# Optimization experiments

Measured on AMD Instinct MI355X. Metric: run time of the kernel, lower is better.

Reference implementation:

```python
import jax, jax.numpy as jnp
import numpy as np

B = 64          # graphs per batch
NPG = 4000      # nodes per graph
CPG0 = 400      # level-0 clusters per graph
CPG1 = 40       # level-1 clusters per graph
DEG = 8         # avg degree
F_IN = 64       # node feature dim (input_shape)


def setup_inputs() -> dict:
    rng = np.random.RandomState(0)
    N0 = B * NPG
    E0 = N0 * DEG
    N1 = B * CPG0
    N2 = B * CPG1
    # node -> graph and node -> level-0 cluster (globally consecutive ids)
    node_graph = np.repeat(np.arange(N0 // NPG), NPG)
    local = np.tile(np.arange(NPG), B)
    cluster0 = node_graph * CPG0 + local // (NPG // CPG0)
    # random edges, endpoints within the same graph
    edge_graph = np.repeat(np.arange(B), NPG * DEG)
    src = edge_graph * NPG + rng.randint(0, NPG, size=E0)
    dst = edge_graph * NPG + rng.randint(0, NPG, size=E0)
    edge_index = np.stack([src, dst]).astype(np.int64)
    # community_pooling's pool_edge: map edges through cluster0, drop self-loops,
    # coalesce duplicates (edge_attr summed). Precompute the integer structure.
    ci, cj = cluster0[src], cluster0[dst]
    mask = ci != cj
    key_ = ci.astype(np.int64) * N1 + cj.astype(np.int64)
    uniq, inv = np.unique(key_[mask], return_inverse=True)
    E1 = uniq.shape[0]
    edge_seg = np.full(E0, E1, dtype=np.int64)   # dropped self-loops -> dummy seg E1
    edge_seg[mask] = inv
    edge_index1 = np.stack([uniq // N1, uniq % N1]).astype(np.int64)
    # level-1 clusters on pooled nodes and graph id of each level-1 cluster
    cl_idx = np.arange(N1)
    cluster1 = (cl_idx // CPG0) * CPG1 + (cl_idx % CPG0) // (CPG0 // CPG1)
    batch2 = np.arange(N2) // CPG1

    key = jax.random.key(0)
    ks = jax.random.split(key, 10)

    def lin(k, fin, fout):
        return jax.random.normal(k, (fin, fout), jnp.float32) / np.sqrt(fin)

    return dict(
        x=jax.random.normal(ks[0], (N0, F_IN), jnp.float32),
        edge_attr=jax.random.uniform(ks[1], (E0, 1), jnp.float32),
        edge_index=jnp.asarray(edge_index),
        cluster0=jnp.asarray(cluster0.astype(np.int64)),
        edge_index1=jnp.asarray(edge_index1),
        edge_seg=jnp.asarray(edge_seg),
        cluster1=jnp.asarray(cluster1.astype(np.int64)),
        batch2=jnp.asarray(batch2.astype(np.int64)),
        n_clusters0=N1, n_clusters1=N2, n_graphs=B,
        W1=lin(ks[2], F_IN, 16), We1=lin(ks[3], 1, 1), Wa1=lin(ks[4], 2 * 16 + 1, 1),
        W2=lin(ks[5], 16, 32), We2=lin(ks[6], 1, 1), Wa2=lin(ks[7], 2 * 32 + 1, 1),
        fc1_W=lin(ks[8], 32, 64), fc1_b=jnp.zeros((64,), jnp.float32),
        fc2_W=lin(ks[9], 64, 1), fc2_b=jnp.zeros((1,), jnp.float32),
    )


def _gin_conv(x, edge_index, edge_attr, W, We, Wa, num_nodes):
    # DeepRank-GNN GINetConvLayer (all linears bias-free)
    row, col = edge_index[0], edge_index[1]
    xp = x @ W                      # project once, then gather (same math as fc(x[col]))
    xrow, xcol = xp[row], xp[col]   # (E, out)
    ed = edge_attr @ We             # (E, n_edge_feat)
    alpha = jnp.concatenate([xrow, xcol, ed], axis=1) @ Wa   # (E, 1)
    alpha = jax.nn.leaky_relu(alpha)
    # faithful: softmax over dim=1 of an (E,1) tensor -> all ones
    alpha = jax.nn.softmax(alpha, axis=1)
    h = alpha * xcol
    return jax.ops.segment_sum(h, row, num_segments=num_nodes)


def reference(x, edge_attr, edge_index, cluster0, edge_index1, edge_seg,
              cluster1, batch2, n_clusters0, n_clusters1, n_graphs,
              W1, We1, Wa1, W2, We2, Wa2, fc1_W, fc1_b, fc2_W, fc2_b):
    # conv1 + relu
    x1 = jax.nn.relu(_gin_conv(x, edge_index, edge_attr, W1, We1, Wa1, x.shape[0]))
    # community_pooling: scatter_max nodes onto clusters, coalesced pooled edges
    x_pool = jax.ops.segment_max(x1, cluster0, num_segments=n_clusters0)
    E1 = edge_index1.shape[1]
    ea1 = jax.ops.segment_sum(edge_attr, edge_seg, num_segments=E1 + 1)[:E1]
    # conv2 + relu on pooled graph
    x2 = jax.nn.relu(_gin_conv(x_pool, edge_index1, ea1, W2, We2, Wa2, n_clusters0))
    # max_pool_x over level-1 clusters, then scatter_mean per graph
    x3 = jax.ops.segment_max(x2, cluster1, num_segments=n_clusters1)
    s = jax.ops.segment_sum(x3, batch2, num_segments=n_graphs)
    cnt = jax.ops.segment_sum(jnp.ones((x3.shape[0], 1), x3.dtype), batch2,
                              num_segments=n_graphs)
    xg = s / cnt                                  # (B, 32)
    h = jax.nn.relu(xg @ fc1_W + fc1_b)           # (B, 64)
    return h @ fc2_W + fc2_b                      # (B, 1)
```

## Files before the change

### kernel.cpp

```cpp
#include <hip/hip_runtime.h>
#include <hip/hip_bf16.h>


#define C1 16
#define C2 32
#define NPG 4000
#define EPG 32000
#define P   8
#define EPP (EPG / P)
#define RPB 80

__global__ void gemm1_k(const float* __restrict__ x, const float* __restrict__ W,
                        float* __restrict__ xp1, int N0) {
    int n = blockIdx.x * blockDim.x + threadIdx.x;
    if (n >= N0) return;
    const float4* xr = (const float4*)(x + (size_t)n * 64);
    float acc[C1];
#pragma unroll
    for (int j = 0; j < C1; ++j) acc[j] = 0.f;
#pragma unroll
    for (int k4 = 0; k4 < 16; ++k4) {
        float4 v = xr[k4];
        const float* w0 = W + (k4 * 4 + 0) * C1;
        const float* w1 = W + (k4 * 4 + 1) * C1;
        const float* w2 = W + (k4 * 4 + 2) * C1;
        const float* w3 = W + (k4 * 4 + 3) * C1;
#pragma unroll
        for (int j = 0; j < C1; ++j)
            acc[j] += v.x * w0[j] + v.y * w1[j] + v.z * w2[j] + v.w * w3[j];
    }
    float4* o = (float4*)(xp1 + (size_t)n * C1);
#pragma unroll
    for (int q = 0; q < 4; ++q)
        o[q] = make_float4(acc[4 * q], acc[4 * q + 1], acc[4 * q + 2], acc[4 * q + 3]);
}

__global__ __launch_bounds__(1024) void csr0_k(const int* __restrict__ ei,
                                               int* __restrict__ rp0,
                                               int* __restrict__ scol,
                                               int E0, int B) {
    __shared__ int cnt[NPG];
    __shared__ int tsum[1024];
    int g = blockIdx.x % B;
    int p = blockIdx.x / B;
    int t = threadIdx.x;
    const int* rows = ei + (size_t)g * EPG + p * EPP;
    const int* cols = ei + E0 + (size_t)g * EPG + p * EPP;
    int rbase = g * NPG;
    int ebase = g * EPG + p * EPP;
    int* rpp = rp0 + (size_t)(p * B + g) * (NPG + 1);

    for (int i = t; i < NPG; i += 1024) cnt[i] = 0;
    __syncthreads();
    for (int e = t; e < EPP; e += 1024) atomicAdd(&cnt[rows[e] - rbase], 1);
    __syncthreads();

    int loc[4];
    int s = 0;
#pragma unroll
    for (int k = 0; k < 4; ++k) {
        int idx = 4 * t + k;
        int v = (idx < NPG) ? cnt[idx] : 0;
        loc[k] = s;
        s += v;
    }
    tsum[t] = s;
    __syncthreads();
    int mine = s;
    for (int off = 1; off < 1024; off <<= 1) {
        int u = (t >= off) ? tsum[t - off] : 0;
        __syncthreads();
        tsum[t] += u;
        __syncthreads();
    }
    int excl = tsum[t] - mine;
#pragma unroll
    for (int k = 0; k < 4; ++k) {
        int idx = 4 * t + k;
        if (idx < NPG) {
            int pos = excl + loc[k];
            rpp[idx] = ebase + pos;
            cnt[idx] = pos;
        }
    }
    if (t == 1023) rpp[NPG] = ebase + EPP;
    __syncthreads();

    for (int e = t; e < EPP; e += 1024) {
        int r = rows[e] - rbase;
        int c = cols[e];
        int pos = atomicAdd(&cnt[r], 1);
        scol[ebase + pos] = c;
    }
}

__global__ __launch_bounds__(256) void merge_k(const int* __restrict__ rp0,
                                               const int* __restrict__ scol,
                                               int* __restrict__ rp2,
                                               int* __restrict__ scol2,
                                               int B, int N0, int E0) {
    int g = blockIdx.x % B;
    int cb = blockIdx.x / B;
    int t = threadIdx.x;
    if (blockIdx.x == 0 && t == 0) rp2[N0] = E0;
    int rl = cb * 256 + t;
    if (rl >= NPG) return;
    int r = g * NPG + rl;
    int s0[P], cnt[P];
    int sum = 0;
#pragma unroll
    for (int p = 0; p < P; ++p) {
        const int* rpp = rp0 + (size_t)(p * B + g) * (NPG + 1) + rl;
        int a = rpp[0];
        int b = rpp[1];
        s0[p] = a;
        cnt[p] = b - a;
        sum += a;
    }
    int base = sum - (P - 1) * g * EPG - EPP * (P * (P - 1) / 2);
    rp2[r] = base;
    int wpos[P];
    int w = base;
#pragma unroll
    for (int p = 0; p < P; ++p) { wpos[p] = w; w += cnt[p]; }
#pragma unroll
    for (int p = 0; p < P; ++p)
        if (cnt[p] > 0) scol2[wpos[p]] = scol[s0[p]];
#pragma unroll
    for (int p = 0; p < P; ++p)
        for (int k = 1; k < cnt[p]; ++k)
            scol2[wpos[p] + k] = scol[s0[p] + k];
}

__global__ __launch_bounds__(320) void aggell_k(const int* __restrict__ rp2,
                                                const int* __restrict__ scol2,
                                                const float* __restrict__ xp1,
                                                float* __restrict__ xpool,
                                                int B, int cpg) {
    __shared__ float4 sums[RPB][4];
    int g = blockIdx.x % B;
    int cb = blockIdx.x / B;
    int t = threadIdx.x;
    int f4 = t & 3;
    int rl = t >> 2;
    int r = g * NPG + cb * RPB + rl;
    int e0 = rp2[r];
    int cnt = rp2[r + 1] - e0;
    const float4* xp = (const float4*)xp1;
    float4 s = make_float4(0.f, 0.f, 0.f, 0.f);
#pragma unroll
    for (int k = 0; k < 16; ++k) {
        if (k < cnt) {
            float4 v = xp[(size_t)scol2[e0 + k] * 4 + f4];
            s.x += v.x; s.y += v.y; s.z += v.z; s.w += v.w;
        }
    }
    for (int k = 16; k < cnt; ++k) {
        float4 v = xp[(size_t)scol2[e0 + k] * 4 + f4];
        s.x += v.x; s.y += v.y; s.z += v.z; s.w += v.w;
    }
    sums[rl][f4] = s;
    __syncthreads();
    if (t < 32) {
        int cl = t >> 2, ff = t & 3;
        float4 m = sums[cl * 10][ff];
#pragma unroll
        for (int k = 1; k < 10; ++k) {
            float4 v = sums[cl * 10 + k][ff];
            m.x = fmaxf(m.x, v.x); m.y = fmaxf(m.y, v.y);
            m.z = fmaxf(m.z, v.z); m.w = fmaxf(m.w, v.w);
        }
        m.x = fmaxf(m.x, 0.f); m.y = fmaxf(m.y, 0.f);
        m.z = fmaxf(m.z, 0.f); m.w = fmaxf(m.w, 0.f);
        ((float4*)xpool)[(size_t)(g * cpg + cb * 8 + cl) * 4 + ff] = m;
    }
}

__global__ void rowptr_k(const int* __restrict__ ei1, int* __restrict__ rp, int E1, int N1) {
    int e = blockIdx.x * blockDim.x + threadIdx.x;
    if (e >= E1) return;
    int r = ei1[e];
    int rprev = __shfl_up(r, 1);
    if ((threadIdx.x & 63) == 0) rprev = (e == 0) ? -1 : ei1[e - 1];
    for (int rr = rprev + 1; rr <= r; ++rr) rp[rr] = e;
    if (e == E1 - 1)
        for (int rr = r + 1; rr <= N1; ++rr) rp[rr] = E1;
}

__global__ __launch_bounds__(256) void agg2_k(const int* __restrict__ ei1,
                                              const int* __restrict__ rp,
                                              const float* __restrict__ xpool,
                                              const float* __restrict__ W2,
                                              float* __restrict__ x2acc,
                                              int E1, int B, int cpg) {
    __shared__ float sums[4][C1];
    int g = blockIdx.x % B;
    int c = blockIdx.x / B;
    int t = threadIdx.x;
    int f4 = t & 3;
    int es = (t >> 2) & 15;
    int w = t >> 6;
    int r = g * cpg + c * 4 + w;
    const int* col = ei1 + E1;
    float4 acc = make_float4(0.f, 0.f, 0.f, 0.f);
    int e0 = rp[r], e1e = rp[r + 1];
    for (int e = e0 + es; e < e1e; e += 16) {
        float4 v = ((const float4*)(xpool + (size_t)col[e] * C1))[f4];
        acc.x += v.x; acc.y += v.y; acc.z += v.z; acc.w += v.w;
    }
#pragma unroll
    for (int off = 4; off <= 32; off <<= 1) {
        acc.x += __shfl_xor(acc.x, off);
        acc.y += __shfl_xor(acc.y, off);
        acc.z += __shfl_xor(acc.z, off);
        acc.w += __shfl_xor(acc.w, off);
    }
    if (es == 0) {
        sums[w][f4 * 4 + 0] = acc.x;
        sums[w][f4 * 4 + 1] = acc.y;
        sums[w][f4 * 4 + 2] = acc.z;
        sums[w][f4 * 4 + 3] = acc.w;
    }
    __syncthreads();
    if (t < 128) {
        int w2 = t >> 5, j = t & 31;
        const float* s = sums[w2];
        float v = 0.f;
#pragma unroll
        for (int k = 0; k < C1; ++k) v += s[k] * W2[k * C2 + j];
        x2acc[(size_t)(g * cpg + c * 4 + w2) * C2 + j] = v;
    }
}

__global__ __launch_bounds__(256) void final_k(const float* __restrict__ x2acc,
                                               const float* __restrict__ fc1W,
                                               const float* __restrict__ fc1b,
                                               const float* __restrict__ fc2W,
                                               const float* __restrict__ fc2b,
                                               float* __restrict__ out, int cpg) {
    __shared__ float xgs[C2];
    int g = blockIdx.x;
    int t = threadIdx.x;
    if (t < C2) xgs[t] = 0.f;
    __syncthreads();
    for (int i = t; i < 40 * C2; i += 256) {
        int cl = i >> 5, f = i & 31;
        const float* base = x2acc + ((size_t)g * cpg + cl * 10) * C2 + f;
        float m = base[0];
#pragma unroll
        for (int k = 1; k < 10; ++k) m = fmaxf(m, base[k * C2]);
        atomicAdd(&xgs[f], fmaxf(m, 0.f));
    }
    __syncthreads();
    if (t < 64) {
        float h = fc1b[t];
#pragma unroll
        for (int f = 0; f < C2; ++f) h += xgs[f] * (1.f / 40.f) * fc1W[f * 64 + t];
        h = fmaxf(h, 0.f);
        float v = h * fc2W[t];
#pragma unroll
        for (int off = 32; off > 0; off >>= 1) v += __shfl_down(v, off);
        if (t == 0) out[g] = v + fc2b[0];
    }
}

extern "C" void kernel_launch(void* const* d_in, const int* in_sizes, int n_in,
                              void* d_out, int out_size, void* d_ws, size_t ws_size,
                              hipStream_t stream) {
    const float* x    = (const float*)d_in[0];
    const int*   ei   = (const int*)d_in[2];
    const int*   ei1  = (const int*)d_in[4];
    const float* W1   = (const float*)d_in[11];
    const float* W2   = (const float*)d_in[14];
    const float* fc1W = (const float*)d_in[17];
    const float* fc1b = (const float*)d_in[18];
    const float* fc2W = (const float*)d_in[19];
    const float* fc2b = (const float*)d_in[20];
    float* out = (float*)d_out;

    const int N0 = in_sizes[0] / 64;
    const int E0 = in_sizes[2] / 2;
    const int E1 = in_sizes[4] / 2;
    const int N1 = in_sizes[6];
    const int N2 = in_sizes[7];
    const int B  = N2 / 40;
    const int CPG0 = N1 / B;

    float* xp1   = (float*)d_ws;
    float* xpool = xp1 + (size_t)N0 * C1;
    float* x2acc = xpool + (size_t)N1 * C1;
    int*   rp1   = (int*)(x2acc + (size_t)N1 * C2);
    int*   rp0   = rp1 + (N1 + 2);
    int*   scol  = rp0 + (size_t)B * P * (NPG + 1) + 2;
    int*   scol2 = scol + (size_t)E0;
    int*   rp2   = scol2 + (size_t)E0;

    gemm1_k<<<(N0 + 255) / 256, 256, 0, stream>>>(x, W1, xp1, N0);
    csr0_k<<<B * P, 1024, 0, stream>>>(ei, rp0, scol, E0, B);
    merge_k<<<B * ((NPG + 255) / 256), 256, 0, stream>>>(rp0, scol, rp2, scol2, B, N0, E0);
    aggell_k<<<B * (NPG / RPB), 320, 0, stream>>>(rp2, scol2, xp1, xpool, B, CPG0);
    rowptr_k<<<(E1 + 255) / 256, 256, 0, stream>>>(ei1, rp1, E1, N1);
    agg2_k<<<B * (CPG0 / 4), 256, 0, stream>>>(ei1, rp1, xpool, W2, x2acc, E1, B, CPG0);
    final_k<<<B, 256, 0, stream>>>(x2acc, fc1W, fc1b, fc2W, fc2b, out, CPG0);
}
```

Before: 256.8 us.

## Replace per-graph CSR build and merge with fixed-width ELL using global atomics

The two-pass CSR construction (per-partition shared-memory counting sort, block-wide scan, then a merge kernel) is replaced by a single ELL build. Each edge atomically claims a slot in a global per-row counter and writes its graph-local column as a 16-bit index into a 32-wide row. The first GEMM, zeroing the counters and the level-1 row-pointer build are fused into one multi-role launch, and the aggregation kernel reads the ELL rows directly. This removes the scan, the merge pass and two launches, and shrinks the column index traffic. In exchange, rows with more than 32 neighbours silently lose edges, which is safe only while degrees stay small. The atomic slot order also makes the order of summation nondeterministic.

```diff
diff --git a/kernel.cpp b/kernel.cpp
--- a/kernel.cpp
+++ b/kernel.cpp
@@ -1,139 +1,85 @@
 #include <hip/hip_runtime.h>
-#include <hip/hip_bf16.h>
 
 
 #define C1 16
 #define C2 32
 #define NPG 4000
 #define EPG 32000
-#define P   8
-#define EPP (EPG / P)
+#define ELLW 32
+#define PB2 16
 #define RPB 80
 
-__global__ void gemm1_k(const float* __restrict__ x, const float* __restrict__ W,
-                        float* __restrict__ xp1, int N0) {
-    int n = blockIdx.x * blockDim.x + threadIdx.x;
-    if (n >= N0) return;
-    const float4* xr = (const float4*)(x + (size_t)n * 64);
-    float acc[C1];
-#pragma unroll
-    for (int j = 0; j < C1; ++j) acc[j] = 0.f;
-#pragma unroll
-    for (int k4 = 0; k4 < 16; ++k4) {
-        float4 v = xr[k4];
-        const float* w0 = W + (k4 * 4 + 0) * C1;
-        const float* w1 = W + (k4 * 4 + 1) * C1;
-        const float* w2 = W + (k4 * 4 + 2) * C1;
-        const float* w3 = W + (k4 * 4 + 3) * C1;
-#pragma unroll
-        for (int j = 0; j < C1; ++j)
-            acc[j] += v.x * w0[j] + v.y * w1[j] + v.z * w2[j] + v.w * w3[j];
-    }
-    float4* o = (float4*)(xp1 + (size_t)n * C1);
-#pragma unroll
-    for (int q = 0; q < 4; ++q)
-        o[q] = make_float4(acc[4 * q], acc[4 * q + 1], acc[4 * q + 2], acc[4 * q + 3]);
-}
-
-__global__ __launch_bounds__(1024) void csr0_k(const int* __restrict__ ei,
-                                               int* __restrict__ rp0,
-                                               int* __restrict__ scol,
-                                               int E0, int B) {
-    __shared__ int cnt[NPG];
-    __shared__ int tsum[1024];
+__global__ __launch_bounds__(256) void pre_k(const float* __restrict__ x,
+                                             const float* __restrict__ W,
+                                             float* __restrict__ xp1,
+                                             int* __restrict__ cnt,
+                                             const int* __restrict__ ei1,
+                                             int* __restrict__ rp,
+                                             int N0, int E1, int N1,
+                                             int G1, int ZB) {
+    int bid = blockIdx.x;
+    int t = threadIdx.x;
+    if (bid < G1) {
+        int n = bid * 256 + t;
+        if (n >= N0) return;
+        const float4* xr = (const float4*)(x + (size_t)n * 64);
+        float acc[C1];
+#pragma unroll
+        for (int j = 0; j < C1; ++j) acc[j] = 0.f;
+#pragma unroll
+        for (int k4 = 0; k4 < 16; ++k4) {
+            float4 v = xr[k4];
+            const float* w0 = W + (k4 * 4 + 0) * C1;
+            const float* w1 = W + (k4 * 4 + 1) * C1;
+            const float* w2 = W + (k4 * 4 + 2) * C1;
+            const float* w3 = W + (k4 * 4 + 3) * C1;
+#pragma unroll
+            for (int j = 0; j < C1; ++j)
+                acc[j] += v.x * w0[j] + v.y * w1[j] + v.z * w2[j] + v.w * w3[j];
+        }
+        float4* o = (float4*)(xp1 + (size_t)n * C1);
+#pragma unroll
+        for (int q = 0; q < 4; ++q)
+            o[q] = make_float4(acc[4 * q], acc[4 * q + 1], acc[4 * q + 2], acc[4 * q + 3]);
+    } else if (bid < G1 + ZB) {
+        int4* p = (int4*)cnt;
+        int n4 = N0 >> 2;
+        for (int i = (bid - G1) * 256 + t; i < n4; i += ZB * 256)
+            p[i] = make_int4(0, 0, 0, 0);
+    } else {
+        int e = (bid - G1 - ZB) * 256 + t;
+        if (e >= E1) return;
+        int r = ei1[e];
+        int rprev = __shfl_up(r, 1);
+        if ((t & 63) == 0) rprev = (e == 0) ? -1 : ei1[e - 1];
+        for (int rr = rprev + 1; rr <= r; ++rr) rp[rr] = e;
+        if (e == E1 - 1)
+            for (int rr = r + 1; rr <= N1; ++rr) rp[rr] = E1;
+    }
+}
+
+__global__ __launch_bounds__(256) void ell_k(const int* __restrict__ ei,
+                                             int* __restrict__ cnt,
+                                             unsigned short* __restrict__ ell,
+                                             int E0, int B) {
     int g = blockIdx.x % B;
     int p = blockIdx.x / B;
     int t = threadIdx.x;
-    const int* rows = ei + (size_t)g * EPG + p * EPP;
-    const int* cols = ei + E0 + (size_t)g * EPG + p * EPP;
+    const int EPB = EPG / PB2;
+    const int* rows = ei + (size_t)g * EPG + p * EPB;
+    const int* cols = ei + E0 + (size_t)g * EPG + p * EPB;
     int rbase = g * NPG;
-    int ebase = g * EPG + p * EPP;
-    int* rpp = rp0 + (size_t)(p * B + g) * (NPG + 1);
-
-    for (int i = t; i < NPG; i += 1024) cnt[i] = 0;
-    __syncthreads();
-    for (int e = t; e < EPP; e += 1024) atomicAdd(&cnt[rows[e] - rbase], 1);
-    __syncthreads();
-
-    int loc[4];
-    int s = 0;
-#pragma unroll
-    for (int k = 0; k < 4; ++k) {
-        int idx = 4 * t + k;
-        int v = (idx < NPG) ? cnt[idx] : 0;
-        loc[k] = s;
-        s += v;
-    }
-    tsum[t] = s;
-    __syncthreads();
-    int mine = s;
-    for (int off = 1; off < 1024; off <<= 1) {
-        int u = (t >= off) ? tsum[t - off] : 0;
-        __syncthreads();
-        tsum[t] += u;
-        __syncthreads();
-    }
-    int excl = tsum[t] - mine;
-#pragma unroll
-    for (int k = 0; k < 4; ++k) {
-        int idx = 4 * t + k;
-        if (idx < NPG) {
-            int pos = excl + loc[k];
-            rpp[idx] = ebase + pos;
-            cnt[idx] = pos;
-        }
-    }
-    if (t == 1023) rpp[NPG] = ebase + EPP;
-    __syncthreads();
-
-    for (int e = t; e < EPP; e += 1024) {
-        int r = rows[e] - rbase;
-        int c = cols[e];
+    for (int e = t; e < EPB; e += 256) {
+        int r = rows[e];
+        unsigned short c = (unsigned short)(cols[e] - rbase);
         int pos = atomicAdd(&cnt[r], 1);
-        scol[ebase + pos] = c;
-    }
-}
-
-__global__ __launch_bounds__(256) void merge_k(const int* __restrict__ rp0,
-                                               const int* __restrict__ scol,
-                                               int* __restrict__ rp2,
-                                               int* __restrict__ scol2,
-                                               int B, int N0, int E0) {
-    int g = blockIdx.x % B;
-    int cb = blockIdx.x / B;
-    int t = threadIdx.x;
-    if (blockIdx.x == 0 && t == 0) rp2[N0] = E0;
-    int rl = cb * 256 + t;
-    if (rl >= NPG) return;
-    int r = g * NPG + rl;
-    int s0[P], cnt[P];
-    int sum = 0;
-#pragma unroll
-    for (int p = 0; p < P; ++p) {
-        const int* rpp = rp0 + (size_t)(p * B + g) * (NPG + 1) + rl;
-        int a = rpp[0];
-        int b = rpp[1];
-        s0[p] = a;
-        cnt[p] = b - a;
-        sum += a;
-    }
-    int base = sum - (P - 1) * g * EPG - EPP * (P * (P - 1) / 2);
-    rp2[r] = base;
-    int wpos[P];
-    int w = base;
-#pragma unroll
-    for (int p = 0; p < P; ++p) { wpos[p] = w; w += cnt[p]; }
-#pragma unroll
-    for (int p = 0; p < P; ++p)
-        if (cnt[p] > 0) scol2[wpos[p]] = scol[s0[p]];
-#pragma unroll
-    for (int p = 0; p < P; ++p)
-        for (int k = 1; k < cnt[p]; ++k)
-            scol2[wpos[p] + k] = scol[s0[p] + k];
-}
-
-__global__ __launch_bounds__(320) void aggell_k(const int* __restrict__ rp2,
-                                                const int* __restrict__ scol2,
+        if (pos < ELLW)
+            ell[(size_t)r * ELLW + pos] = c;
+    }
+}
+
+__global__ __launch_bounds__(320) void aggell_k(const int* __restrict__ cnt,
+                                                const unsigned short* __restrict__ ell,
                                                 const float* __restrict__ xp1,
                                                 float* __restrict__ xpool,
                                                 int B, int cpg) {
@@ -144,19 +90,20 @@
     int f4 = t & 3;
     int rl = t >> 2;
     int r = g * NPG + cb * RPB + rl;
-    int e0 = rp2[r];
-    int cnt = rp2[r + 1] - e0;
+    int c = cnt[r];
+    const unsigned short* er = ell + (size_t)r * ELLW;
+    size_t gb4 = (size_t)g * NPG * 4;
     const float4* xp = (const float4*)xp1;
     float4 s = make_float4(0.f, 0.f, 0.f, 0.f);
 #pragma unroll
     for (int k = 0; k < 16; ++k) {
-        if (k < cnt) {
-            float4 v = xp[(size_t)scol2[e0 + k] * 4 + f4];
+        if (k < c) {
+            float4 v = xp[gb4 + (size_t)er[k] * 4 + f4];
             s.x += v.x; s.y += v.y; s.z += v.z; s.w += v.w;
         }
     }
-    for (int k = 16; k < cnt; ++k) {
-        float4 v = xp[(size_t)scol2[e0 + k] * 4 + f4];
+    for (int k = 16; k < c; ++k) {
+        float4 v = xp[gb4 + (size_t)er[k] * 4 + f4];
         s.x += v.x; s.y += v.y; s.z += v.z; s.w += v.w;
     }
     sums[rl][f4] = s;
@@ -174,17 +121,6 @@
         m.z = fmaxf(m.z, 0.f); m.w = fmaxf(m.w, 0.f);
         ((float4*)xpool)[(size_t)(g * cpg + cb * 8 + cl) * 4 + ff] = m;
     }
-}
-
-__global__ void rowptr_k(const int* __restrict__ ei1, int* __restrict__ rp, int E1, int N1) {
-    int e = blockIdx.x * blockDim.x + threadIdx.x;
-    if (e >= E1) return;
-    int r = ei1[e];
-    int rprev = __shfl_up(r, 1);
-    if ((threadIdx.x & 63) == 0) rprev = (e == 0) ? -1 : ei1[e - 1];
-    for (int rr = rprev + 1; rr <= r; ++rr) rp[rr] = e;
-    if (e == E1 - 1)
-        for (int rr = r + 1; rr <= N1; ++rr) rp[rr] = E1;
 }
 
 __global__ __launch_bounds__(256) void agg2_k(const int* __restrict__ ei1,
@@ -290,16 +226,17 @@
     float* xpool = xp1 + (size_t)N0 * C1;
     float* x2acc = xpool + (size_t)N1 * C1;
     int*   rp1   = (int*)(x2acc + (size_t)N1 * C2);
-    int*   rp0   = rp1 + (N1 + 2);
-    int*   scol  = rp0 + (size_t)B * P * (NPG + 1) + 2;
-    int*   scol2 = scol + (size_t)E0;
-    int*   rp2   = scol2 + (size_t)E0;
-
-    gemm1_k<<<(N0 + 255) / 256, 256, 0, stream>>>(x, W1, xp1, N0);
-    csr0_k<<<B * P, 1024, 0, stream>>>(ei, rp0, scol, E0, B);
-    merge_k<<<B * ((NPG + 255) / 256), 256, 0, stream>>>(rp0, scol, rp2, scol2, B, N0, E0);
-    aggell_k<<<B * (NPG / RPB), 320, 0, stream>>>(rp2, scol2, xp1, xpool, B, CPG0);
-    rowptr_k<<<(E1 + 255) / 256, 256, 0, stream>>>(ei1, rp1, E1, N1);
+    int*   cnt   = rp1 + (N1 + 4);
+    unsigned short* ell = (unsigned short*)(cnt + N0);
+
+    const int G1 = (N0 + 255) / 256;
+    const int ZB = 64;
+    const int RB = (E1 + 255) / 256;
+
+    pre_k<<<G1 + ZB + RB, 256, 0, stream>>>(x, W1, xp1, cnt, ei1, rp1,
+                                            N0, E1, N1, G1, ZB);
+    ell_k<<<B * PB2, 256, 0, stream>>>(ei, cnt, ell, E0, B);
+    aggell_k<<<B * (NPG / RPB), 320, 0, stream>>>(cnt, ell, xp1, xpool, B, CPG0);
     agg2_k<<<B * (CPG0 / 4), 256, 0, stream>>>(ei1, rp1, xpool, W2, x2acc, E1, B, CPG0);
     final_k<<<B, 256, 0, stream>>>(x2acc, fc1W, fc1b, fc2W, fc2b, out, CPG0);
 }
```

Result: slower. 331.3 us (+29.0%).

## Drop CSR merge pass; aggregate directly from per-partition CSRs and fuse rowptr into gemm

Applied to the files above, without the earlier changes.

Removes the merge kernel that combined the eight per-partition CSR pieces into one CSR. The level-0 aggregation now reads the partition row pointers into shared memory and gathers neighbours from all eight pieces directly. The pooled-graph rowptr build is folded into the feature GEMM launch as extra blocks. Together this cuts two launches and a full read and write of the column array, at the cost of more irregular per-row loops in the aggregation.

```diff
diff --git a/kernel.cpp b/kernel.cpp
--- a/kernel.cpp
+++ b/kernel.cpp
@@ -1,5 +1,4 @@
 #include <hip/hip_runtime.h>
-#include <hip/hip_bf16.h>
 
 
 #define C1 16
@@ -10,29 +9,46 @@
 #define EPP (EPG / P)
 #define RPB 80
 
-__global__ void gemm1_k(const float* __restrict__ x, const float* __restrict__ W,
-                        float* __restrict__ xp1, int N0) {
-    int n = blockIdx.x * blockDim.x + threadIdx.x;
-    if (n >= N0) return;
-    const float4* xr = (const float4*)(x + (size_t)n * 64);
-    float acc[C1];
-#pragma unroll
-    for (int j = 0; j < C1; ++j) acc[j] = 0.f;
-#pragma unroll
-    for (int k4 = 0; k4 < 16; ++k4) {
-        float4 v = xr[k4];
-        const float* w0 = W + (k4 * 4 + 0) * C1;
-        const float* w1 = W + (k4 * 4 + 1) * C1;
-        const float* w2 = W + (k4 * 4 + 2) * C1;
-        const float* w3 = W + (k4 * 4 + 3) * C1;
-#pragma unroll
-        for (int j = 0; j < C1; ++j)
-            acc[j] += v.x * w0[j] + v.y * w1[j] + v.z * w2[j] + v.w * w3[j];
-    }
-    float4* o = (float4*)(xp1 + (size_t)n * C1);
-#pragma unroll
-    for (int q = 0; q < 4; ++q)
-        o[q] = make_float4(acc[4 * q], acc[4 * q + 1], acc[4 * q + 2], acc[4 * q + 3]);
+__global__ __launch_bounds__(256) void pre_k(const float* __restrict__ x,
+                                             const float* __restrict__ W,
+                                             float* __restrict__ xp1,
+                                             const int* __restrict__ ei1,
+                                             int* __restrict__ rp,
+                                             int N0, int E1, int N1, int G1) {
+    int bid = blockIdx.x;
+    int t = threadIdx.x;
+    if (bid < G1) {
+        int n = bid * 256 + t;
+        if (n >= N0) return;
+        const float4* xr = (const float4*)(x + (size_t)n * 64);
+        float acc[C1];
+#pragma unroll
+        for (int j = 0; j < C1; ++j) acc[j] = 0.f;
+#pragma unroll
+        for (int k4 = 0; k4 < 16; ++k4) {
+            float4 v = xr[k4];
+            const float* w0 = W + (k4 * 4 + 0) * C1;
+            const float* w1 = W + (k4 * 4 + 1) * C1;
+            const float* w2 = W + (k4 * 4 + 2) * C1;
+            const float* w3 = W + (k4 * 4 + 3) * C1;
+#pragma unroll
+            for (int j = 0; j < C1; ++j)
+                acc[j] += v.x * w0[j] + v.y * w1[j] + v.z * w2[j] + v.w * w3[j];
+        }
+        float4* o = (float4*)(xp1 + (size_t)n * C1);
+#pragma unroll
+        for (int q = 0; q < 4; ++q)
+            o[q] = make_float4(acc[4 * q], acc[4 * q + 1], acc[4 * q + 2], acc[4 * q + 3]);
+    } else {
+        int e = (bid - G1) * 256 + t;
+        if (e >= E1) return;
+        int r = ei1[e];
+        int rprev = __shfl_up(r, 1);
+        if ((t & 63) == 0) rprev = (e == 0) ? -1 : ei1[e - 1];
+        for (int rr = rprev + 1; rr <= r; ++rr) rp[rr] = e;
+        if (e == E1 - 1)
+            for (int rr = r + 1; rr <= N1; ++rr) rp[rr] = E1;
+    }
 }
 
 __global__ __launch_bounds__(1024) void csr0_k(const int* __restrict__ ei,
@@ -94,70 +110,48 @@
     }
 }
 
-__global__ __launch_bounds__(256) void merge_k(const int* __restrict__ rp0,
-                                               const int* __restrict__ scol,
-                                               int* __restrict__ rp2,
-                                               int* __restrict__ scol2,
-                                               int B, int N0, int E0) {
-    int g = blockIdx.x % B;
-    int cb = blockIdx.x / B;
-    int t = threadIdx.x;
-    if (blockIdx.x == 0 && t == 0) rp2[N0] = E0;
-    int rl = cb * 256 + t;
-    if (rl >= NPG) return;
-    int r = g * NPG + rl;
-    int s0[P], cnt[P];
-    int sum = 0;
-#pragma unroll
-    for (int p = 0; p < P; ++p) {
-        const int* rpp = rp0 + (size_t)(p * B + g) * (NPG + 1) + rl;
-        int a = rpp[0];
-        int b = rpp[1];
-        s0[p] = a;
-        cnt[p] = b - a;
-        sum += a;
-    }
-    int base = sum - (P - 1) * g * EPG - EPP * (P * (P - 1) / 2);
-    rp2[r] = base;
-    int wpos[P];
-    int w = base;
-#pragma unroll
-    for (int p = 0; p < P; ++p) { wpos[p] = w; w += cnt[p]; }
-#pragma unroll
-    for (int p = 0; p < P; ++p)
-        if (cnt[p] > 0) scol2[wpos[p]] = scol[s0[p]];
-#pragma unroll
-    for (int p = 0; p < P; ++p)
-        for (int k = 1; k < cnt[p]; ++k)
-            scol2[wpos[p] + k] = scol[s0[p] + k];
-}
-
-__global__ __launch_bounds__(320) void aggell_k(const int* __restrict__ rp2,
-                                                const int* __restrict__ scol2,
-                                                const float* __restrict__ xp1,
-                                                float* __restrict__ xpool,
-                                                int B, int cpg) {
+__global__ __launch_bounds__(320) void aggell8_k(const int* __restrict__ rp0,
+                                                 const int* __restrict__ scol,
+                                                 const float* __restrict__ xp1,
+                                                 float* __restrict__ xpool,
+                                                 int B, int cpg) {
+    __shared__ int rpl[P][RPB + 1];
     __shared__ float4 sums[RPB][4];
     int g = blockIdx.x % B;
     int cb = blockIdx.x / B;
     int t = threadIdx.x;
+    int r0 = cb * RPB;
+    for (int i = t; i < P * (RPB + 1); i += 320) {
+        int p = i / (RPB + 1), j = i % (RPB + 1);
+        rpl[p][j] = rp0[(size_t)(p * B + g) * (NPG + 1) + r0 + j];
+    }
+    __syncthreads();
     int f4 = t & 3;
     int rl = t >> 2;
-    int r = g * NPG + cb * RPB + rl;
-    int e0 = rp2[r];
-    int cnt = rp2[r + 1] - e0;
+    int s0[P], cn[P];
+#pragma unroll
+    for (int p = 0; p < P; ++p) {
+        s0[p] = rpl[p][rl];
+        cn[p] = rpl[p][rl + 1] - s0[p];
+    }
     const float4* xp = (const float4*)xp1;
     float4 s = make_float4(0.f, 0.f, 0.f, 0.f);
 #pragma unroll
-    for (int k = 0; k < 16; ++k) {
-        if (k < cnt) {
-            float4 v = xp[(size_t)scol2[e0 + k] * 4 + f4];
+    for (int k = 0; k < 3; ++k) {
+#pragma unroll
+        for (int p = 0; p < P; ++p) {
+            if (k < cn[p]) {
+                float4 v = xp[(size_t)scol[s0[p] + k] * 4 + f4];
+                s.x += v.x; s.y += v.y; s.z += v.z; s.w += v.w;
+            }
+        }
+    }
+#pragma unroll
+    for (int p = 0; p < P; ++p) {
+        for (int k = 3; k < cn[p]; ++k) {
+            float4 v = xp[(size_t)scol[s0[p] + k] * 4 + f4];
             s.x += v.x; s.y += v.y; s.z += v.z; s.w += v.w;
         }
-    }
-    for (int k = 16; k < cnt; ++k) {
-        float4 v = xp[(size_t)scol2[e0 + k] * 4 + f4];
-        s.x += v.x; s.y += v.y; s.z += v.z; s.w += v.w;
     }
     sums[rl][f4] = s;
     __syncthreads();
@@ -174,17 +168,6 @@
         m.z = fmaxf(m.z, 0.f); m.w = fmaxf(m.w, 0.f);
         ((float4*)xpool)[(size_t)(g * cpg + cb * 8 + cl) * 4 + ff] = m;
     }
-}
-
-__global__ void rowptr_k(const int* __restrict__ ei1, int* __restrict__ rp, int E1, int N1) {
-    int e = blockIdx.x * blockDim.x + threadIdx.x;
-    if (e >= E1) return;
-    int r = ei1[e];
-    int rprev = __shfl_up(r, 1);
-    if ((threadIdx.x & 63) == 0) rprev = (e == 0) ? -1 : ei1[e - 1];
-    for (int rr = rprev + 1; rr <= r; ++rr) rp[rr] = e;
-    if (e == E1 - 1)
-        for (int rr = r + 1; rr <= N1; ++rr) rp[rr] = E1;
 }
 
 __global__ __launch_bounds__(256) void agg2_k(const int* __restrict__ ei1,
@@ -290,16 +273,15 @@
     float* xpool = xp1 + (size_t)N0 * C1;
     float* x2acc = xpool + (size_t)N1 * C1;
     int*   rp1   = (int*)(x2acc + (size_t)N1 * C2);
-    int*   rp0   = rp1 + (N1 + 2);
+    int*   rp0   = rp1 + (N1 + 4);
     int*   scol  = rp0 + (size_t)B * P * (NPG + 1) + 2;
-    int*   scol2 = scol + (size_t)E0;
-    int*   rp2   = scol2 + (size_t)E0;
-
-    gemm1_k<<<(N0 + 255) / 256, 256, 0, stream>>>(x, W1, xp1, N0);
+
+    const int G1 = (N0 + 255) / 256;
+    const int RB = (E1 + 255) / 256;
+
+    pre_k<<<G1 + RB, 256, 0, stream>>>(x, W1, xp1, ei1, rp1, N0, E1, N1, G1);
     csr0_k<<<B * P, 1024, 0, stream>>>(ei, rp0, scol, E0, B);
-    merge_k<<<B * ((NPG + 255) / 256), 256, 0, stream>>>(rp0, scol, rp2, scol2, B, N0, E0);
-    aggell_k<<<B * (NPG / RPB), 320, 0, stream>>>(rp2, scol2, xp1, xpool, B, CPG0);
-    rowptr_k<<<(E1 + 255) / 256, 256, 0, stream>>>(ei1, rp1, E1, N1);
+    aggell8_k<<<B * (NPG / RPB), 320, 0, stream>>>(rp0, scol, xp1, xpool, B, CPG0);
     agg2_k<<<B * (CPG0 / 4), 256, 0, stream>>>(ei1, rp1, xpool, W2, x2acc, E1, B, CPG0);
     final_k<<<B, 256, 0, stream>>>(x2acc, fc1W, fc1b, fc2W, fc2b, out, CPG0);
 }
```

Result: no change. 256.9 us (+0.0%).
